# Kernel optimization log

Measured on AMD Instinct MI355X. Metric: run time of the kernel, lower is better.

The kernel has to match this reference:

```python
import jax, jax.numpy as jnp
import numpy as np

PLANES = 512
HEADS = 8            # factorization(512) -> largest divisor < 10 is 8
DIM_HEAD = PLANES // HEADS
B, N = 4, 1024
EPS = 1e-5


def _layernorm(x, g, b):
    mu = jnp.mean(x, axis=-1, keepdims=True)
    var = jnp.mean((x - mu) ** 2, axis=-1, keepdims=True)
    return (x - mu) * jax.lax.rsqrt(var + EPS) * g + b


def _split_heads(t, b, n):
    # einops 'b n (d h) -> b h n d'  (head index is the FAST axis of the split)
    return t.reshape(b, n, DIM_HEAD, HEADS).transpose(0, 3, 1, 2)


def _tlayer(x, mask, wqkv, bqkv, g1, be1, w1, b1, w2, b2, g2, be2):
    b, n, d = x.shape
    qkv = x @ wqkv + bqkv                      # [b, n, 3*planes]
    q, k, v = jnp.split(qkv, 3, axis=-1)
    q, k, v = _split_heads(q, b, n), _split_heads(k, b, n), _split_heads(v, b, n)
    q = q / jnp.sqrt(jnp.float32(d))           # NOTE: source divides by sqrt(planes), not sqrt(dim_head)
    dots = jnp.einsum('bhid,bhjd->bhij', q, k) + mask
    attn = jax.nn.softmax(dots, axis=-1)
    out = jnp.einsum('bhij,bhjd->bhid', attn, v)
    out = out.transpose(0, 2, 1, 3).reshape(b, n, d)   # 'b h n d -> b n (h d)'
    x = _layernorm(x + out, g1, be1)
    ff = jax.nn.gelu(x @ w1 + b1, approximate=False) @ w2 + b2
    return _layernorm(x + ff, g2, be2)


def setup_inputs() -> dict:
    key = jax.random.key(0)
    ks = iter(jax.random.split(key, 40))
    s = 0.02
    inp = {"x": jax.random.normal(next(ks), (B, N, PLANES), jnp.float32)}
    for L in (1, 2):
        inp[f"wqkv{L}"] = jax.random.normal(next(ks), (PLANES, 3 * PLANES), jnp.float32) * s
        inp[f"bqkv{L}"] = jnp.zeros((3 * PLANES,), jnp.float32)
        inp[f"g{L}a"] = jnp.ones((PLANES,), jnp.float32)
        inp[f"be{L}a"] = jnp.zeros((PLANES,), jnp.float32)
        inp[f"w{L}1"] = jax.random.normal(next(ks), (PLANES, PLANES), jnp.float32) * s
        inp[f"b{L}1"] = jnp.zeros((PLANES,), jnp.float32)
        inp[f"w{L}2"] = jax.random.normal(next(ks), (PLANES, PLANES), jnp.float32) * s
        inp[f"b{L}2"] = jnp.zeros((PLANES,), jnp.float32)
        inp[f"g{L}b"] = jnp.ones((PLANES,), jnp.float32)
        inp[f"be{L}b"] = jnp.zeros((PLANES,), jnp.float32)
    return inp


def reference(x, wqkv1, bqkv1, g1a, be1a, w11, b11, w12, b12, g1b, be1b,
              wqkv2, bqkv2, g2a, be2a, w21, b21, w22, b22, g2b, be2b):
    n = x.shape[1]
    neg = jnp.full((n, n), -jnp.inf, jnp.float32)
    tril_mask = jnp.triu(neg, 1)    # -inf strictly above diagonal (causal)
    triu_mask = jnp.tril(neg, -1)   # -inf strictly below diagonal (anti-causal)
    td1 = jax.nn.sigmoid(_tlayer(x, tril_mask, wqkv1, bqkv1, g1a, be1a, w11, b11, w12, b12, g1b, be1b))
    td2 = jax.nn.sigmoid(_tlayer(x, triu_mask, wqkv2, bqkv2, g2a, be2a, w21, b21, w22, b22, g2b, be2b))
    sim = jnp.einsum('bnd,bmd->bnm', td1, td2) / td1.shape[-1]
    return sim
```

## Files before the change

kernel.cpp:

```cpp
#include <hip/hip_runtime.h>
#include <math.h>


typedef float f32x4 __attribute__((ext_vector_type(4)));
typedef short s16x8 __attribute__((ext_vector_type(8)));
typedef int   i32x4 __attribute__((ext_vector_type(4)));
typedef unsigned short u16;
typedef unsigned int u32;

#define NTOK 1024
#define PL 512
#define QSCALE 0.04419417382415922f

__device__ inline u16 f2bf(float f) {
    unsigned u = __builtin_bit_cast(unsigned, f);
    unsigned r = u + 0x7fffu + ((u >> 16) & 1u);
    return (u16)(r >> 16);
}
__device__ inline float bf2f(u16 h) {
    unsigned u = ((unsigned)h) << 16;
    return __builtin_bit_cast(float, u);
}
__device__ inline u32 cvtpk(float a, float b) {
    u32 r;
    asm("v_cvt_pk_bf16_f32 %0, %1, %2" : "=v"(r) : "v"(a), "v"(b));
    return r;
}

__device__ inline void gll16(const void* g, void* l) {
    __builtin_amdgcn_global_load_lds(
        (const __attribute__((address_space(1))) u32*)g,
        (__attribute__((address_space(3))) u32*)l, 16, 0, 0);
}

__global__ __launch_bounds__(256) void prep(const float* __restrict__ X,
    u16* __restrict__ xhi,
    const float* __restrict__ Wq0, const float* __restrict__ Wq1, u16* __restrict__ wqh,
    const float* __restrict__ W10, const float* __restrict__ W11, u16* __restrict__ w1h,
    const float* __restrict__ W20, const float* __restrict__ W21, u16* __restrict__ w2h)
{
    const int bid = blockIdx.x;
    if (bid < 2048) {
        const int i = (bid * 256 + threadIdx.x) * 4;
        float4 v = *(const float4*)&X[i];
        xhi[i + 0] = f2bf(v.x); xhi[i + 1] = f2bf(v.y);
        xhi[i + 2] = f2bf(v.z); xhi[i + 3] = f2bf(v.w);
        return;
    }
    const float* W;
    u16* Whi;
    int N, kx, ny;
    if (bid < 3584) {
        const int idx = bid - 2048;
        const int z = idx / 768, rem = idx % 768;
        kx = rem % 16; ny = rem / 16;
        W = z ? Wq1 : Wq0; Whi = wqh + (size_t)z * 786432; N = 1536;
    } else if (bid < 4096) {
        const int idx = bid - 3584;
        const int z = idx / 256, rem = idx % 256;
        kx = rem % 16; ny = rem / 16;
        W = z ? W11 : W10; Whi = w1h + (size_t)z * 262144; N = 512;
    } else {
        const int idx = bid - 4096;
        const int z = idx / 256, rem = idx % 256;
        kx = rem % 16; ny = rem / 16;
        W = z ? W21 : W20; Whi = w2h + (size_t)z * 262144; N = 512;
    }
    __shared__ float T[32][36];
    const int k0 = kx * 32, n0 = ny * 32;
    const int tr = threadIdx.x >> 3, tc = (threadIdx.x & 7) * 4;
    *(float4*)&T[tr][tc] = *(const float4*)&W[(size_t)(k0 + tr) * N + n0 + tc];
    __syncthreads();
    const size_t o = (size_t)(n0 + tr) * 512 + k0 + tc;
    #pragma unroll
    for (int j = 0; j < 4; j++) Whi[o + j] = f2bf(T[tc + j][tr]);
}

__device__ inline int qkv_perm(int j) {
    return (j >> 9) * 512 + ((j & 63) << 3) + ((j >> 6) & 7);
}

template<int BM, int EPI>
__global__ __launch_bounds__(256) void gemm_mfma(
    const u16* __restrict__ AB, const size_t aLS,
    const u16* __restrict__ BB, const size_t bLS,
    const float* __restrict__ bias0, const float* __restrict__ bias1, const int Ncols,
    u16* __restrict__ oh0, u16* __restrict__ oh1)
{
    constexpr int FM = BM / 32;
    constexpr int WMS = BM / 2;
    __shared__ u16 Ah[2][BM * 32], Bh[2][128 * 32];
    const int z = blockIdx.z;
    const u16* A = AB + (size_t)z * aLS;
    const u16* B = BB + (size_t)z * bLS;
    const float* bias = z ? bias1 : bias0;
    u16* oh = z ? oh1 : oh0;

    const int t = threadIdx.x, l = t & 63, w = t >> 6;
    const int lr = l & 15, lg = l >> 4;
    const int wm = w >> 1, wn = w & 1;
    const int m0 = blockIdx.x * BM, n0 = blockIdx.y * 128;
    const int srow = l >> 2, sch = l & 3;

    f32x4 acc[FM][4];
    #pragma unroll
    for (int i = 0; i < FM; i++)
        #pragma unroll
        for (int j = 0; j < 4; j++) acc[i][j] = f32x4{0.f, 0.f, 0.f, 0.f};

    auto stage = [&](int bufi, int k0) {
        for (int j = w; j < BM / 16; j += 4) {
            const int r = j * 16 + srow;
            const int ck = sch ^ ((r >> 1) & 3);
            gll16(&A[(size_t)(m0 + r) * 512 + k0 + ck * 8], &Ah[bufi][j * 512]);
        }
        for (int j = w; j < 8; j += 4) {
            const int r = j * 16 + srow;
            const int ck = sch ^ ((r >> 1) & 3);
            const int brow = (EPI == 0) ? qkv_perm(n0 + r) : (n0 + r);
            gll16(&B[(size_t)brow * 512 + k0 + ck * 8], &Bh[bufi][j * 512]);
        }
    };

    stage(0, 0);
    __syncthreads();
    int buf = 0;
    for (int kt = 0; kt < 16; kt++) {
        if (kt < 15) stage(buf ^ 1, (kt + 1) * 32);

        s16x8 ah[FM];
        #pragma unroll
        for (int fm = 0; fm < FM; fm++) {
            const int r = wm * WMS + fm * 16 + lr;
            ah[fm] = *(const s16x8*)&Ah[buf][r * 32 + ((lg ^ ((r >> 1) & 3)) << 3)];
        }
        #pragma unroll
        for (int fn = 0; fn < 4; fn++) {
            const int r = wn * 64 + fn * 16 + lr;
            s16x8 bh = *(const s16x8*)&Bh[buf][r * 32 + ((lg ^ ((r >> 1) & 3)) << 3)];
            #pragma unroll
            for (int fm = 0; fm < FM; fm++)
                acc[fm][fn] = __builtin_amdgcn_mfma_f32_16x16x32_bf16(ah[fm], bh, acc[fm][fn], 0, 0, 0);
        }
        __syncthreads();
        buf ^= 1;
    }
    #pragma unroll
    for (int fm = 0; fm < FM; fm++)
        #pragma unroll
        for (int fn = 0; fn < 4; fn++)
            #pragma unroll
            for (int rg = 0; rg < 4; rg++) {
                const int r = m0 + wm * WMS + fm * 16 + lg * 4 + rg;
                const int c = n0 + wn * 64 + fn * 16 + lr;
                if constexpr (EPI == 0) {
                    float v = acc[fm][fn][rg] + bias[qkv_perm(c)];
                    if (c < 512) v *= QSCALE;
                    oh[((size_t)z * 4096 + r) * Ncols + c] = f2bf(v);
                } else {
                    float gl = acc[fm][fn][rg] + bias[c];
                    if constexpr (EPI == 1)
                        gl = 0.5f * gl * (1.f + erff(gl * 0.70710678118654752f));
                    oh[(size_t)r * Ncols + c] = f2bf(gl);
                }
            }
}

__global__ __launch_bounds__(256) void attn_mfma(const u16* __restrict__ QKV,
    u16* __restrict__ AO0, u16* __restrict__ AO1)
{
    __shared__ u16 Ks[2][64 * 64];
    __shared__ u16 Vs[2][64 * 64];
    const int t = threadIdx.x, l = t & 63, w = t >> 6;
    const int lr = l & 15, lg = l >> 4;
    const int z = blockIdx.z;
    const int causal = (z == 0);
    const int bh = blockIdx.x;
    const int b = bh >> 3, h = bh & 7;
    const int qt = causal ? (15 - (int)blockIdx.y) : (int)blockIdx.y;
    const u16* base = QKV + ((size_t)z * 4096 + (size_t)b * NTOK) * 1536;
    u16* AO = z ? AO1 : AO0;
    const int q0 = qt * 64 + w * 16;

    s16x8 aq[2];
    aq[0] = *(const s16x8*)&base[(size_t)(q0 + lr) * 1536 + h * 64 + lg * 8];
    aq[1] = *(const s16x8*)&base[(size_t)(q0 + lr) * 1536 + h * 64 + 32 + lg * 8];

    f32x4 o[4];
    float m_ = -INFINITY, l_ = 0.f;
    #pragma unroll
    for (int f = 0; f < 4; f++) o[f] = f32x4{0.f, 0.f, 0.f, 0.f};

    const int kt0 = causal ? 0 : qt, kt1 = causal ? qt : 15;

    auto stageK = [&](int kt) {
        #pragma unroll
        for (int i = 0; i < 2; i++) {
            const int j = w * 2 + i;
            const int r = j * 8 + (l >> 3);
            const int ck = (l & 7) ^ (r & 7);
            gll16(&base[(size_t)(kt * 64 + r) * 1536 + 512 + h * 64 + ck * 8],
                  &Ks[kt & 1][j * 512]);
        }
    };
    const int jv = t & 63;
    s16x8 va, vb;
    auto loadV = [&](int kt) {
        const u16* vr = &base[(size_t)(kt * 64 + jv) * 1536 + 1024 + h * 64 + w * 16];
        va = *(const s16x8*)&vr[0];
        vb = *(const s16x8*)&vr[8];
    };
    auto writeV = [&](int kt) {
        #pragma unroll
        for (int i = 0; i < 8; i++) {
            const int d = w * 16 + i;
            Vs[kt & 1][d * 64 + (((jv >> 3) ^ (d & 7)) << 3) + (jv & 7)] = (u16)va[i];
        }
        #pragma unroll
        for (int i = 0; i < 8; i++) {
            const int d = w * 16 + 8 + i;
            Vs[kt & 1][d * 64 + (((jv >> 3) ^ (d & 7)) << 3) + (jv & 7)] = (u16)vb[i];
        }
    };

    s16x8 pap[2];
    float psc[4] = {1.f, 1.f, 1.f, 1.f};
    int pneed = 1;

    auto QK = [&](int kt, f32x4* s) {
        #pragma unroll
        for (int f = 0; f < 4; f++) s[f] = f32x4{0.f, 0.f, 0.f, 0.f};
        #pragma unroll
        for (int kk = 0; kk < 2; kk++)
            #pragma unroll
            for (int f = 0; f < 4; f++) {
                const int row = f * 16 + lr;
                const int ch = kk * 4 + lg;
                s16x8 bk = *(const s16x8*)&Ks[kt & 1][row * 64 + ((ch ^ (row & 7)) << 3)];
                s[f] = __builtin_amdgcn_mfma_f32_16x16x32_bf16(bk, aq[kk], s[f], 0, 0, 0);
            }
        if (kt == qt) {
            const int q = q0 + lr;
            #pragma unroll
            for (int f = 0; f < 4; f++)
                #pragma unroll
                for (int r = 0; r < 4; r++) {
                    const int key = kt * 64 + f * 16 + lg * 4 + r;
                    if (causal ? (key > q) : (key < q)) s[f][r] = -INFINITY;
                }
        }
    };

    auto SM = [&](f32x4* s) {
        float rm = s[0][0];
        #pragma unroll
        for (int f = 0; f < 4; f++)
            #pragma unroll
            for (int r = 0; r < 4; r++) rm = fmaxf(rm, s[f][r]);
        rm = fmaxf(rm, __shfl_xor(rm, 16));
        rm = fmaxf(rm, __shfl_xor(rm, 32));
        pneed = !__all(rm <= m_ + 8.f);
        const float mn = pneed ? fmaxf(m_, rm) : m_;
        const float sc = __expf(m_ - mn);
        float ps = 0.f;
        #pragma unroll
        for (int f = 0; f < 4; f++)
            #pragma unroll
            for (int r = 0; r < 4; r++) {
                float p = __expf(s[f][r] - mn);
                s[f][r] = p;
                ps += p;
            }
        ps += __shfl_xor(ps, 16);
        ps += __shfl_xor(ps, 32);
        l_ = l_ * sc + ps;
        m_ = mn;
        u32 P01[4], P23[4];
        #pragma unroll
        for (int f = 0; f < 4; f++) {
            P01[f] = cvtpk(s[f][0], s[f][1]);
            P23[f] = cvtpk(s[f][2], s[f][3]);
        }
        const int srcA = lr + ((lg & 1) << 5);
        const int srcB = srcA + 16;
        #pragma unroll
        for (int kk = 0; kk < 2; kk++) {
            const u32 a01_0 = (u32)__shfl((int)P01[2 * kk], srcA);
            const u32 a01_1 = (u32)__shfl((int)P01[2 * kk + 1], srcA);
            const u32 a23_0 = (u32)__shfl((int)P23[2 * kk], srcA);
            const u32 a23_1 = (u32)__shfl((int)P23[2 * kk + 1], srcA);
            const u32 b01_0 = (u32)__shfl((int)P01[2 * kk], srcB);
            const u32 b01_1 = (u32)__shfl((int)P01[2 * kk + 1], srcB);
            const u32 b23_0 = (u32)__shfl((int)P23[2 * kk], srcB);
            const u32 b23_1 = (u32)__shfl((int)P23[2 * kk + 1], srcB);
            i32x4 av;
            av[0] = (int)((lg & 2) ? a01_1 : a01_0);
            av[1] = (int)((lg & 2) ? a23_1 : a23_0);
            av[2] = (int)((lg & 2) ? b01_1 : b01_0);
            av[3] = (int)((lg & 2) ? b23_1 : b23_0);
            pap[kk] = __builtin_bit_cast(s16x8, av);
        }
        if (pneed) {
            #pragma unroll
            for (int r = 0; r < 4; r++) psc[r] = __shfl(sc, lg * 4 + r);
        }
    };

    auto PV = [&](int kt) {
        if (pneed) {
            #pragma unroll
            for (int r = 0; r < 4; r++)
                #pragma unroll
                for (int f = 0; f < 4; f++) o[f][r] *= psc[r];
        }
        #pragma unroll
        for (int kk = 0; kk < 2; kk++)
            #pragma unroll
            for (int f = 0; f < 4; f++) {
                const int row = f * 16 + lr;
                const int ch = kk * 4 + lg;
                s16x8 bv = *(const s16x8*)&Vs[kt & 1][row * 64 + ((ch ^ (row & 7)) << 3)];
                o[f] = __builtin_amdgcn_mfma_f32_16x16x32_bf16(pap[kk], bv, o[f], 0, 0, 0);
            }
    };

    stageK(kt0);
    if (kt0 < kt1) stageK(kt0 + 1);
    loadV(kt0);
    writeV(kt0);
    __syncthreads();
    {
        f32x4 s0[4];
        QK(kt0, s0);
        SM(s0);
    }
    __syncthreads();

    for (int kt = kt0; kt <= kt1; kt++) {
        if (kt + 2 <= kt1) stageK(kt + 2);
        if (kt + 1 <= kt1) loadV(kt + 1);
        f32x4 sn[4];
        __builtin_amdgcn_s_setprio(1);
        if (kt + 1 <= kt1) QK(kt + 1, sn);
        PV(kt);
        __builtin_amdgcn_s_setprio(0);
        if (kt + 1 <= kt1) {
            SM(sn);
            writeV(kt + 1);
        }
        __syncthreads();
    }

    const float linv = 1.f / l_;
    #pragma unroll
    for (int r = 0; r < 4; r++) {
        const float lv = __shfl(linv, lg * 4 + r);
        #pragma unroll
        for (int f = 0; f < 4; f++)
            AO[(size_t)(b * NTOK + q0 + lg * 4 + r) * PL + h * 64 + f * 16 + lr] =
                f2bf(o[f][r] * lv);
    }
}

__global__ __launch_bounds__(256) void add_ln_a(const float* __restrict__ X,
    const u16* __restrict__ A0, const u16* __restrict__ A1,
    const float* __restrict__ g0, const float* __restrict__ g1,
    const float* __restrict__ be0, const float* __restrict__ be1,
    u16* __restrict__ OB, const size_t oLS)
{
    const int z = blockIdx.z;
    const u16* A = z ? A1 : A0;
    const float* g = z ? g1 : g0;
    const float* be = z ? be1 : be0;
    u16* O = OB + (size_t)z * oLS;
    const int row = blockIdx.x * 4 + (threadIdx.x >> 6);
    const int lane = threadIdx.x & 63;
    const float* xr = X + (size_t)row * PL;
    const u16* ar = A + (size_t)row * PL;
    float v[8];
    float sum = 0.f;
    #pragma unroll
    for (int u = 0; u < 8; u++) { v[u] = xr[lane + u * 64] + bf2f(ar[lane + u * 64]); sum += v[u]; }
    #pragma unroll
    for (int o = 32; o > 0; o >>= 1) sum += __shfl_xor(sum, o);
    const float mu = sum * (1.f / 512.f);
    float s2 = 0.f;
    #pragma unroll
    for (int u = 0; u < 8; u++) { float d = v[u] - mu; s2 = fmaf(d, d, s2); }
    #pragma unroll
    for (int o = 32; o > 0; o >>= 1) s2 += __shfl_xor(s2, o);
    const float rstd = rsqrtf(s2 * (1.f / 512.f) + 1e-5f);
    #pragma unroll
    for (int u = 0; u < 8; u++) {
        const int c = lane + u * 64;
        O[(size_t)row * PL + c] = f2bf((v[u] - mu) * rstd * g[c] + be[c]);
    }
}

__global__ __launch_bounds__(256) void add_ln_b(
    const u16* __restrict__ X1B, const size_t xLS,
    const u16* __restrict__ FB, const size_t fLS,
    const float* __restrict__ g0, const float* __restrict__ g1,
    const float* __restrict__ be0, const float* __restrict__ be1,
    u16* __restrict__ TDB, const size_t tLS)
{
    const int z = blockIdx.z;
    const u16* X1 = X1B + (size_t)z * xLS;
    const u16* F = FB + (size_t)z * fLS;
    const float* g = z ? g1 : g0;
    const float* be = z ? be1 : be0;
    u16* TD = TDB + (size_t)z * tLS;
    const int row = blockIdx.x * 4 + (threadIdx.x >> 6);
    const int lane = threadIdx.x & 63;
    const size_t ro = (size_t)row * PL;
    float v[8];
    float sum = 0.f;
    #pragma unroll
    for (int u = 0; u < 8; u++) {
        const int c = lane + u * 64;
        v[u] = bf2f(X1[ro + c]) + bf2f(F[ro + c]);
        sum += v[u];
    }
    #pragma unroll
    for (int o = 32; o > 0; o >>= 1) sum += __shfl_xor(sum, o);
    const float mu = sum * (1.f / 512.f);
    float s2 = 0.f;
    #pragma unroll
    for (int u = 0; u < 8; u++) { float d = v[u] - mu; s2 = fmaf(d, d, s2); }
    #pragma unroll
    for (int o = 32; o > 0; o >>= 1) s2 += __shfl_xor(s2, o);
    const float rstd = rsqrtf(s2 * (1.f / 512.f) + 1e-5f);
    #pragma unroll
    for (int u = 0; u < 8; u++) {
        const int c = lane + u * 64;
        float y = (v[u] - mu) * rstd * g[c] + be[c];
        TD[ro + c] = f2bf(1.f / (1.f + expf(-y)));
    }
}

__global__ __launch_bounds__(256) void sim_mfma(const u16* __restrict__ TD1,
    const u16* __restrict__ TD2, float* __restrict__ Out)
{
    __shared__ u16 Ah[2][64 * 64], Bh[2][128 * 64];
    const int t = threadIdx.x, l = t & 63, w = t >> 6;
    const int lr = l & 15, lg = l >> 4;
    const int wm = w >> 1, wn = w & 1;
    const int bz = blockIdx.z;
    const u16* A = TD1 + (size_t)bz * NTOK * PL;
    const u16* B = TD2 + (size_t)bz * NTOK * PL;
    const int m0 = blockIdx.x * 64, n0 = blockIdx.y * 128;

    f32x4 acc[2][4];
    #pragma unroll
    for (int i = 0; i < 2; i++)
        #pragma unroll
        for (int j = 0; j < 4; j++) acc[i][j] = f32x4{0.f, 0.f, 0.f, 0.f};

    auto stage = [&](int bufi, int k0) {
        #pragma unroll
        for (int i = 0; i < 2; i++) {
            const int j = w * 2 + i;
            const int r = j * 8 + (l >> 3);
            const int ck = (l & 7) ^ (r & 7);
            gll16(&A[(size_t)(m0 + r) * 512 + k0 + ck * 8], &Ah[bufi][j * 512]);
        }
        #pragma unroll
        for (int i = 0; i < 4; i++) {
            const int j = w * 4 + i;
            const int r = j * 8 + (l >> 3);
            const int ck = (l & 7) ^ (r & 7);
            gll16(&B[(size_t)(n0 + r) * 512 + k0 + ck * 8], &Bh[bufi][j * 512]);
        }
    };

    stage(0, 0);
    __syncthreads();
    int buf = 0;
    for (int kt = 0; kt < 8; kt++) {
        if (kt < 7) stage(buf ^ 1, (kt + 1) * 64);
        #pragma unroll
        for (int kk = 0; kk < 2; kk++) {
            const int ch = kk * 4 + lg;
            s16x8 af[2], bf[4];
            #pragma unroll
            for (int fm = 0; fm < 2; fm++) {
                const int r = wm * 32 + fm * 16 + lr;
                af[fm] = *(const s16x8*)&Ah[buf][r * 64 + ((ch ^ (r & 7)) << 3)];
            }
            #pragma unroll
            for (int fn = 0; fn < 4; fn++) {
                const int r = wn * 64 + fn * 16 + lr;
                bf[fn] = *(const s16x8*)&Bh[buf][r * 64 + ((ch ^ (r & 7)) << 3)];
            }
            #pragma unroll
            for (int fm = 0; fm < 2; fm++)
                #pragma unroll
                for (int fn = 0; fn < 4; fn++)
                    acc[fm][fn] = __builtin_amdgcn_mfma_f32_16x16x32_bf16(af[fm], bf[fn], acc[fm][fn], 0, 0, 0);
        }
        __syncthreads();
        buf ^= 1;
    }
    #pragma unroll
    for (int fm = 0; fm < 2; fm++)
        #pragma unroll
        for (int fn = 0; fn < 4; fn++)
            #pragma unroll
            for (int rg = 0; rg < 4; rg++) {
                const int r = m0 + wm * 32 + fm * 16 + lg * 4 + rg;
                const int c = n0 + wn * 64 + fn * 16 + lr;
                Out[((size_t)(bz * NTOK + r)) * NTOK + c] = acc[fm][fn][rg] * (1.f / 512.f);
            }
}

extern "C" void kernel_launch(void* const* d_in, const int* in_sizes, int n_in,
                              void* d_out, int out_size, void* d_ws, size_t ws_size,
                              hipStream_t stream)
{
    const float* x = (const float*)d_in[0];
    const float* wqkv[2] = {(const float*)d_in[1],  (const float*)d_in[11]};
    const float* bqkv[2] = {(const float*)d_in[2],  (const float*)d_in[12]};
    const float* ga[2]   = {(const float*)d_in[3],  (const float*)d_in[13]};
    const float* bea[2]  = {(const float*)d_in[4],  (const float*)d_in[14]};
    const float* w1[2]   = {(const float*)d_in[5],  (const float*)d_in[15]};
    const float* b1[2]   = {(const float*)d_in[6],  (const float*)d_in[16]};
    const float* w2[2]   = {(const float*)d_in[7],  (const float*)d_in[17]};
    const float* b2[2]   = {(const float*)d_in[8],  (const float*)d_in[18]};
    const float* gb[2]   = {(const float*)d_in[9],  (const float*)d_in[19]};
    const float* beb[2]  = {(const float*)d_in[10], (const float*)d_in[20]};

    char* wsb = (char*)d_ws;
    char* ob  = (char*)d_out;
    #define WSK(kb) ((char*)wsb + ((size_t)(kb) << 10))
    #define OBK(kb) ((char*)ob  + ((size_t)(kb) << 10))
    u16* xhi = (u16*)WSK(0);
    u16* x1  = (u16*)WSK(0);
    u16* wqh = (u16*)WSK(8192);
    u16* td1 = (u16*)WSK(8192);
    u16* td2 = (u16*)WSK(12288);
    u16* w1h = (u16*)WSK(11264);
    u16* w2h = (u16*)WSK(12288);
    u16* qkvB = (u16*)WSK(13312);
    u16* ffo = (u16*)WSK(24576);
    u16* AO0 = (u16*)OBK(0);
    u16* AO1 = (u16*)OBK(4096);
    u16* hB  = (u16*)OBK(8192);
    float* out = (float*)d_out;

    prep<<<4608, 256, 0, stream>>>(x, xhi,
        wqkv[0], wqkv[1], wqh, w1[0], w1[1], w1h, w2[0], w2[1], w2h);
    gemm_mfma<128, 0><<<dim3(32, 12, 2), 256, 0, stream>>>(
        xhi, 0, wqh, 786432, bqkv[0], bqkv[1], 1536,
        qkvB, qkvB);
    attn_mfma<<<dim3(32, 16, 2), 256, 0, stream>>>(qkvB, AO0, AO1);
    add_ln_a<<<dim3(1024, 1, 2), 256, 0, stream>>>(x, AO0, AO1,
        ga[0], ga[1], bea[0], bea[1], x1, 2097152);
    gemm_mfma<64, 1><<<dim3(64, 4, 2), 256, 0, stream>>>(
        x1, 2097152, w1h, 262144, b1[0], b1[1], 512,
        hB, hB + 2097152);
    gemm_mfma<64, 2><<<dim3(64, 4, 2), 256, 0, stream>>>(
        hB, 2097152, w2h, 262144, b2[0], b2[1], 512,
        ffo, ffo + 2097152);
    add_ln_b<<<dim3(1024, 1, 2), 256, 0, stream>>>(
        x1, 2097152, ffo, 2097152,
        gb[0], gb[1], beb[0], beb[1], td1, 2097152);
    sim_mfma<<<dim3(16, 8, 4), 256, 0, stream>>>(td1, td2, out);
}
```

Measured before the change: 125.8 us.

## Process 128 query rows per attention block with two fragments per wave

The attention kernel now gives each block a 128-row query tile, with every wave handling two 16-row fragments, each keeping its own online-softmax state. Each K/V tile staged in shared memory is therefore reused by twice as many queries, cutting global K/V traffic and staging work per query. The grid shrinks to half as many blocks, and per-wave register pressure rises from the doubled accumulators, so parallelism and occupancy drop and causal load imbalance gets coarser. The running max now starts at 0 rather than minus infinity, relying on scores being small enough for the deferred-rescale logic to stay correct.

New measurement: 136.7 us. 8.7% more time.

```diff
diff --git a/kernel.cpp b/kernel.cpp
--- a/kernel.cpp
+++ b/kernel.cpp
@@ -177,21 +177,28 @@
     const int causal = (z == 0);
     const int bh = blockIdx.x;
     const int b = bh >> 3, h = bh & 7;
-    const int qt = causal ? (15 - (int)blockIdx.y) : (int)blockIdx.y;
+    const int qt = causal ? (7 - (int)blockIdx.y) : (int)blockIdx.y;
     const u16* base = QKV + ((size_t)z * 4096 + (size_t)b * NTOK) * 1536;
     u16* AO = z ? AO1 : AO0;
-    const int q0 = qt * 64 + w * 16;
-
-    s16x8 aq[2];
-    aq[0] = *(const s16x8*)&base[(size_t)(q0 + lr) * 1536 + h * 64 + lg * 8];
-    aq[1] = *(const s16x8*)&base[(size_t)(q0 + lr) * 1536 + h * 64 + 32 + lg * 8];
-
-    f32x4 o[4];
-    float m_ = -INFINITY, l_ = 0.f;
-    #pragma unroll
-    for (int f = 0; f < 4; f++) o[f] = f32x4{0.f, 0.f, 0.f, 0.f};
-
-    const int kt0 = causal ? 0 : qt, kt1 = causal ? qt : 15;
+    const int q0 = qt * 128 + w * 32;
+
+    s16x8 aq[2][2];
+    #pragma unroll
+    for (int qf = 0; qf < 2; qf++) {
+        aq[qf][0] = *(const s16x8*)&base[(size_t)(q0 + qf * 16 + lr) * 1536 + h * 64 + lg * 8];
+        aq[qf][1] = *(const s16x8*)&base[(size_t)(q0 + qf * 16 + lr) * 1536 + h * 64 + 32 + lg * 8];
+    }
+
+    f32x4 o[2][4];
+    float m_[2] = {0.f, 0.f};
+    float l_[2] = {0.f, 0.f};
+    #pragma unroll
+    for (int qf = 0; qf < 2; qf++)
+        #pragma unroll
+        for (int f = 0; f < 4; f++) o[qf][f] = f32x4{0.f, 0.f, 0.f, 0.f};
+
+    const int kt0 = causal ? 0 : 2 * qt;
+    const int kt1 = causal ? (2 * qt + 1) : 15;
 
     auto stageK = [&](int kt) {
         #pragma unroll
@@ -223,11 +230,11 @@
         }
     };
 
-    s16x8 pap[2];
-    float psc[4] = {1.f, 1.f, 1.f, 1.f};
-    int pneed = 1;
-
-    auto QK = [&](int kt, f32x4* s) {
+    s16x8 pap[2][2];
+    float psc[2][4] = {{1.f,1.f,1.f,1.f},{1.f,1.f,1.f,1.f}};
+    int pneed[2] = {0, 0};
+
+    auto QK = [&](int kt, int qf, f32x4* s) {
         #pragma unroll
         for (int f = 0; f < 4; f++) s[f] = f32x4{0.f, 0.f, 0.f, 0.f};
         #pragma unroll
@@ -237,10 +244,11 @@
                 const int row = f * 16 + lr;
                 const int ch = kk * 4 + lg;
                 s16x8 bk = *(const s16x8*)&Ks[kt & 1][row * 64 + ((ch ^ (row & 7)) << 3)];
-                s[f] = __builtin_amdgcn_mfma_f32_16x16x32_bf16(bk, aq[kk], s[f], 0, 0, 0);
-            }
-        if (kt == qt) {
-            const int q = q0 + lr;
+                s[f] = __builtin_amdgcn_mfma_f32_16x16x32_bf16(bk, aq[qf][kk], s[f], 0, 0, 0);
+            }
+        const int needMask = causal ? (kt >= 2 * qt) : (kt <= 2 * qt + 1);
+        if (needMask) {
+            const int q = q0 + qf * 16 + lr;
             #pragma unroll
             for (int f = 0; f < 4; f++)
                 #pragma unroll
@@ -251,7 +259,7 @@
         }
     };
 
-    auto SM = [&](f32x4* s) {
+    auto SM = [&](int qf, f32x4* s) {
         float rm = s[0][0];
         #pragma unroll
         for (int f = 0; f < 4; f++)
@@ -259,9 +267,9 @@
             for (int r = 0; r < 4; r++) rm = fmaxf(rm, s[f][r]);
         rm = fmaxf(rm, __shfl_xor(rm, 16));
         rm = fmaxf(rm, __shfl_xor(rm, 32));
-        pneed = !__all(rm <= m_ + 8.f);
-        const float mn = pneed ? fmaxf(m_, rm) : m_;
-        const float sc = __expf(m_ - mn);
+        pneed[qf] = !__all(rm <= m_[qf] + 8.f);
+        const float mn = pneed[qf] ? fmaxf(m_[qf], rm) : m_[qf];
+        const float sc = __expf(m_[qf] - mn);
         float ps = 0.f;
         #pragma unroll
         for (int f = 0; f < 4; f++)
@@ -273,8 +281,8 @@
             }
         ps += __shfl_xor(ps, 16);
         ps += __shfl_xor(ps, 32);
-        l_ = l_ * sc + ps;
-        m_ = mn;
+        l_[qf] = l_[qf] * sc + ps;
+        m_[qf] = mn;
         u32 P01[4], P23[4];
         #pragma unroll
         for (int f = 0; f < 4; f++) {
@@ -298,20 +306,20 @@
             av[1] = (int)((lg & 2) ? a23_1 : a23_0);
             av[2] = (int)((lg & 2) ? b01_1 : b01_0);
             av[3] = (int)((lg & 2) ? b23_1 : b23_0);
-            pap[kk] = __builtin_bit_cast(s16x8, av);
-        }
-        if (pneed) {
-            #pragma unroll
-            for (int r = 0; r < 4; r++) psc[r] = __shfl(sc, lg * 4 + r);
-        }
-    };
-
-    auto PV = [&](int kt) {
-        if (pneed) {
+            pap[qf][kk] = __builtin_bit_cast(s16x8, av);
+        }
+        if (pneed[qf]) {
+            #pragma unroll
+            for (int r = 0; r < 4; r++) psc[qf][r] = __shfl(sc, lg * 4 + r);
+        }
+    };
+
+    auto PV = [&](int kt, int qf) {
+        if (pneed[qf]) {
             #pragma unroll
             for (int r = 0; r < 4; r++)
                 #pragma unroll
-                for (int f = 0; f < 4; f++) o[f][r] *= psc[r];
+                for (int f = 0; f < 4; f++) o[qf][f][r] *= psc[qf][r];
         }
         #pragma unroll
         for (int kk = 0; kk < 2; kk++)
@@ -320,19 +328,21 @@
                 const int row = f * 16 + lr;
                 const int ch = kk * 4 + lg;
                 s16x8 bv = *(const s16x8*)&Vs[kt & 1][row * 64 + ((ch ^ (row & 7)) << 3)];
-                o[f] = __builtin_amdgcn_mfma_f32_16x16x32_bf16(pap[kk], bv, o[f], 0, 0, 0);
+                o[qf][f] = __builtin_amdgcn_mfma_f32_16x16x32_bf16(pap[qf][kk], bv, o[qf][f], 0, 0, 0);
             }
     };
 
     stageK(kt0);
-    if (kt0 < kt1) stageK(kt0 + 1);
+    stageK(kt0 + 1);
     loadV(kt0);
     writeV(kt0);
     __syncthreads();
     {
         f32x4 s0[4];
-        QK(kt0, s0);
-        SM(s0);
+        QK(kt0, 0, s0);
+        SM(0, s0);
+        QK(kt0, 1, s0);
+        SM(1, s0);
     }
     __syncthreads();
 
@@ -341,24 +351,30 @@
         if (kt + 1 <= kt1) loadV(kt + 1);
         f32x4 sn[4];
         __builtin_amdgcn_s_setprio(1);
-        if (kt + 1 <= kt1) QK(kt + 1, sn);
-        PV(kt);
+        if (kt + 1 <= kt1) QK(kt + 1, 0, sn);
+        PV(kt, 0);
+        if (kt + 1 <= kt1) SM(0, sn);
+        if (kt + 1 <= kt1) QK(kt + 1, 1, sn);
+        PV(kt, 1);
         __builtin_amdgcn_s_setprio(0);
         if (kt + 1 <= kt1) {
-            SM(sn);
+            SM(1, sn);
             writeV(kt + 1);
         }
         __syncthreads();
     }
 
-    const float linv = 1.f / l_;
-    #pragma unroll
-    for (int r = 0; r < 4; r++) {
-        const float lv = __shfl(linv, lg * 4 + r);
-        #pragma unroll
-        for (int f = 0; f < 4; f++)
-            AO[(size_t)(b * NTOK + q0 + lg * 4 + r) * PL + h * 64 + f * 16 + lr] =
-                f2bf(o[f][r] * lv);
+    #pragma unroll
+    for (int qf = 0; qf < 2; qf++) {
+        const float linv = 1.f / l_[qf];
+        #pragma unroll
+        for (int r = 0; r < 4; r++) {
+            const float lv = __shfl(linv, lg * 4 + r);
+            #pragma unroll
+            for (int f = 0; f < 4; f++)
+                AO[(size_t)(b * NTOK + q0 + qf * 16 + lg * 4 + r) * PL + h * 64 + f * 16 + lr] =
+                    f2bf(o[qf][f][r] * lv);
+        }
     }
 }
 
@@ -552,7 +568,7 @@
     gemm_mfma<128, 0><<<dim3(32, 12, 2), 256, 0, stream>>>(
         xhi, 0, wqh, 786432, bqkv[0], bqkv[1], 1536,
         qkvB, qkvB);
-    attn_mfma<<<dim3(32, 16, 2), 256, 0, stream>>>(qkvB, AO0, AO1);
+    attn_mfma<<<dim3(32, 8, 2), 256, 0, stream>>>(qkvB, AO0, AO1);
     add_ln_a<<<dim3(1024, 1, 2), 256, 0, stream>>>(x, AO0, AO1,
         ga[0], ga[1], bea[0], bea[1], x1, 2097152);
     gemm_mfma<64, 1><<<dim3(64, 4, 2), 256, 0, stream>>>(
```
